# Optimization experiments

Measured on AMD Instinct MI355X. Metric: run time of the kernel, lower is better.

The kernel has to match this reference:

```python
import math
import jax, jax.numpy as jnp
import numpy as np

B, N, M, D, P, H, DH, L, FI = 4, 1024, 512, 512, 256, 8, 64, 6, 2048
ROT_DIM = 32          # min(32, dim_head)
NUM_BUCKETS, MAX_DIST = 32, 128


def layer_norm(x, g, stable=False, eps=1e-5):
    if stable:
        x = x / jax.lax.stop_gradient(jnp.max(x, axis=-1, keepdims=True))
    mu = jnp.mean(x, axis=-1, keepdims=True)
    var = jnp.mean(jnp.square(x - mu), axis=-1, keepdims=True)
    return (x - mu) * jax.lax.rsqrt(var + eps) * g


def rel_pos_bias(emb, i, j):
    # T5-style buckets for causal relative positions; emb: [NUM_BUCKETS, H]
    rel = jnp.arange(j)[None, :] - jnp.arange(i)[:, None]
    n = jnp.maximum(-rel, 0)
    max_exact = NUM_BUCKETS // 2
    nf = jnp.maximum(n, 1).astype(jnp.float32)
    large = max_exact + (jnp.log(nf / max_exact) / math.log(MAX_DIST / max_exact) * (NUM_BUCKETS - max_exact)).astype(jnp.int32)
    bucket = jnp.where(n < max_exact, n, jnp.minimum(large, NUM_BUCKETS - 1))
    return jnp.transpose(emb[bucket], (2, 0, 1))  # [h, i, j]


def rotary_pos(n):
    inv = 1.0 / (10000.0 ** (jnp.arange(0, ROT_DIM, 2, dtype=jnp.float32) / ROT_DIM))
    f = jnp.arange(n, dtype=jnp.float32)[:, None] * inv[None, :]
    return jnp.concatenate([f, f], axis=-1)  # [n, ROT_DIM]


def apply_rotary(pos, t):
    r = pos.shape[-1]
    t_rot, t_pass = t[..., :r], t[..., r:]
    x1, x2 = jnp.split(t_rot, 2, axis=-1)
    t_rot = t_rot * jnp.cos(pos) + jnp.concatenate([-x2, x1], axis=-1) * jnp.sin(pos)
    return jnp.concatenate([t_rot, t_pass], axis=-1)


def attention(x, kv_inp, norm_g, ctx_g, wq, wkv, null_kv, wo, out_g,
              attn_bias=None, causal=False, rot=None):
    b, n, _ = x.shape
    xn = layer_norm(x, norm_g)
    kv_in = xn if kv_inp is None else layer_norm(kv_inp, ctx_g)
    q = (xn @ wq).reshape(b, n, H, DH).transpose(0, 2, 1, 3)   # b h n d
    k, v = jnp.split(kv_in @ wkv, 2, axis=-1)                  # b m d (single-head kv)
    q = q * (DH ** -0.5)
    if rot is not None:
        q = apply_rotary(rot, q)
        k = apply_rotary(rot, k)
    k = jnp.concatenate([jnp.broadcast_to(null_kv[0], (b, 1, DH)), k], axis=1)
    v = jnp.concatenate([jnp.broadcast_to(null_kv[1], (b, 1, DH)), v], axis=1)
    sim = jnp.einsum('bhid,bjd->bhij', q, k)
    if attn_bias is not None:
        sim = sim + attn_bias
    if causal:
        i, j = sim.shape[-2], sim.shape[-1]
        mask = jnp.triu(jnp.ones((i, j), dtype=bool), j - i + 1)  # null token always visible
        sim = jnp.where(mask, jnp.finfo(sim.dtype).min, sim)
    attn = jax.nn.softmax(sim, axis=-1)
    out = jnp.einsum('bhij,bjd->bhid', attn, v).transpose(0, 2, 1, 3).reshape(b, n, H * DH)
    return layer_norm(out @ wo, out_g)


def feed_forward(x, g, w1, w2):
    h, gate = jnp.split(layer_norm(x, g) @ w1, 2, axis=-1)  # SwiGLU
    return (h * jax.nn.silu(gate)) @ w2


def _forward(x, context, rel_emb, sa_norm_g, sa_wq, sa_wkv, sa_null_kv, sa_wo, sa_out_g,
             ca_norm_g, ca_ctx_g, ca_wq, ca_wkv, ca_null_kv, ca_wo, ca_out_g,
             ff_norm_g, ff_w1, ff_w2, norm_g):
    n = x.shape[1]
    attn_bias = rel_pos_bias(rel_emb, n, n + 1)
    rot = rotary_pos(n)
    for l in range(sa_wq.shape[0]):
        x = attention(x, None, sa_norm_g[l], None, sa_wq[l], sa_wkv[l], sa_null_kv[l],
                      sa_wo[l], sa_out_g[l], attn_bias=attn_bias, causal=True, rot=rot) + x
        x = attention(x, context, ca_norm_g[l], ca_ctx_g[l], ca_wq[l], ca_wkv[l],
                      ca_null_kv[l], ca_wo[l], ca_out_g[l]) + x
        x = feed_forward(x, ff_norm_g[l], ff_w1[l], ff_w2[l]) + x
    return layer_norm(x, norm_g, stable=True)


def setup_inputs() -> dict:
    key = jax.random.key(0)
    ks = jax.random.split(key, 16)
    ID = H * DH
    r = lambda i, shape: jax.random.normal(ks[i], shape, jnp.float32) * 0.02
    return dict(
        x=jax.random.normal(ks[0], (B, N, D), jnp.float32),
        context=jax.random.normal(ks[1], (B, M, P), jnp.float32),
        rel_emb=r(2, (NUM_BUCKETS, H)),
        sa_norm_g=jnp.ones((L, D)), sa_wq=r(3, (L, D, ID)), sa_wkv=r(4, (L, D, 2 * DH)),
        sa_null_kv=r(5, (L, 2, DH)), sa_wo=r(6, (L, ID, D)), sa_out_g=jnp.ones((L, D)),
        ca_norm_g=jnp.ones((L, D)), ca_ctx_g=jnp.ones((L, P)), ca_wq=r(7, (L, D, ID)),
        ca_wkv=r(8, (L, P, 2 * DH)), ca_null_kv=r(9, (L, 2, DH)), ca_wo=r(10, (L, ID, D)),
        ca_out_g=jnp.ones((L, D)),
        ff_norm_g=jnp.ones((L, D)), ff_w1=r(11, (L, D, 2 * FI)), ff_w2=r(12, (L, FI, D)),
        norm_g=jnp.ones((D,)),
    )


def reference(x, context, rel_emb, sa_norm_g, sa_wq, sa_wkv, sa_null_kv, sa_wo, sa_out_g,
              ca_norm_g, ca_ctx_g, ca_wq, ca_wkv, ca_null_kv, ca_wo, ca_out_g,
              ff_norm_g, ff_w1, ff_w2, norm_g):
    return _forward(x, context, rel_emb, sa_norm_g, sa_wq, sa_wkv, sa_null_kv, sa_wo, sa_out_g,
                    ca_norm_g, ca_ctx_g, ca_wq, ca_wkv, ca_null_kv, ca_wo, ca_out_g,
                    ff_norm_g, ff_w1, ff_w2, norm_g)
```

## Files before the change

### kernel.cpp

```cpp
#include <hip/hip_runtime.h>
#include <hip/hip_bf16.h>
#include <math.h>

#define BB 4
#define NN 1024
#define MM 512
#define DD 512
#define PP 256
#define HH 8
#define DHH 64
#define LL 6
#define FFI 2048

typedef unsigned short u16;
typedef __attribute__((ext_vector_type(8))) short frag8;
typedef __attribute__((ext_vector_type(4))) float f32x4;

__device__ __forceinline__ u16 f2bf(float f) {
  union { float f; unsigned u; } x; x.f = f;
  unsigned u = x.u;
  return (u16)((u + 0x7FFFu + ((u >> 16) & 1u)) >> 16);
}

__global__ __launch_bounds__(256) void ln_kernel(const float* __restrict__ x,
                                                 const float* __restrict__ g,
                                                 const float* __restrict__ resid,
                                                 void* __restrict__ y,
                                                 int cols, int stable, int obf) {
  __shared__ float sbuf[8];
  int row = blockIdx.x;
  const float* xr = x + (size_t)row * cols;
  int tid = threadIdx.x;

  float inv_mx = 1.f;
  if (stable) {
    float mx = -INFINITY;
    for (int c = tid; c < cols; c += 256) mx = fmaxf(mx, xr[c]);
    #pragma unroll
    for (int o = 32; o > 0; o >>= 1) mx = fmaxf(mx, __shfl_xor(mx, o));
    if ((tid & 63) == 0) sbuf[tid >> 6] = mx;
    __syncthreads();
    mx = fmaxf(fmaxf(sbuf[0], sbuf[1]), fmaxf(sbuf[2], sbuf[3]));
    __syncthreads();
    inv_mx = 1.f / mx;
  }

  float sum = 0.f, ss = 0.f;
  for (int c = tid; c < cols; c += 256) {
    float v = xr[c] * inv_mx;
    sum += v; ss += v * v;
  }
  #pragma unroll
  for (int o = 32; o > 0; o >>= 1) { sum += __shfl_xor(sum, o); ss += __shfl_xor(ss, o); }
  if ((tid & 63) == 0) { sbuf[tid >> 6] = sum; sbuf[4 + (tid >> 6)] = ss; }
  __syncthreads();
  sum = sbuf[0] + sbuf[1] + sbuf[2] + sbuf[3];
  ss  = sbuf[4] + sbuf[5] + sbuf[6] + sbuf[7];

  float mean = sum / cols;
  float var  = ss / cols - mean * mean;
  float r = rsqrtf(var + 1e-5f);
  for (int c = tid; c < cols; c += 256) {
    float v = (xr[c] * inv_mx - mean) * r * g[c];
    if (resid) v += resid[(size_t)row * cols + c];
    if (obf) ((u16*)y)[(size_t)row * cols + c] = f2bf(v);
    else     ((float*)y)[(size_t)row * cols + c] = v;
  }
}

__global__ __launch_bounds__(256) void wtrans_kernel(const float* __restrict__ W,
                                                     u16* __restrict__ Wt,
                                                     int K, int N) {
  __shared__ float tile[32][33];
  size_t lofs = (size_t)blockIdx.z * K * N;
  const float* Wl = W + lofs;
  u16* Wtl = Wt + lofs;
  int n0 = blockIdx.x * 32, k0 = blockIdx.y * 32;
  int t = threadIdx.x;
  #pragma unroll
  for (int it = 0; it < 4; it++) {
    int idx = t + it * 256;
    int r = idx >> 5, c = idx & 31;
    tile[r][c] = Wl[(size_t)(k0 + r) * N + n0 + c];
  }
  __syncthreads();
  #pragma unroll
  for (int it = 0; it < 4; it++) {
    int idx = t + it * 256;
    int r = idx >> 5, c = idx & 31;
    Wtl[(size_t)(n0 + r) * K + k0 + c] = f2bf(tile[c][r]);
  }
}

#define LSTR 40

template<int TM, int TN, int RES>
__global__ __launch_bounds__(256) void mfma_gemm(const u16* __restrict__ A,
                                                 const u16* __restrict__ Bt,
                                                 float* __restrict__ C,
                                                 const float* __restrict__ res,
                                                 int M, int N, int K) {
  constexpr int TM2 = TM / 2, TN2 = TN / 2;
  constexpr int IT = TM2 / 16, JT = TN2 / 16;
  constexpr int ASLOT = TM * 4 / 256, BSLOT = TN * 4 / 256;
  __shared__ u16 As[TM * LSTR];
  __shared__ u16 Bs[TN * LSTR];
  int t = threadIdx.x;
  int w = t >> 6, lane = t & 63;
  int bm = blockIdx.y * TM, bn = blockIdx.x * TN;
  int wr = (w >> 1) * TM2, wc = (w & 1) * TN2;
  int lm = lane & 15, q = lane >> 4;

  f32x4 acc[IT][JT] = {};

  for (int k0 = 0; k0 < K; k0 += 32) {
    __syncthreads();
    #pragma unroll
    for (int i = 0; i < ASLOT; i++) {
      int s = t + i * 256; int m = s >> 2, c = s & 3;
      uint4 d = *(const uint4*)(A + (size_t)(bm + m) * K + k0 + c * 8);
      *(uint4*)&As[m * LSTR + c * 8] = d;
    }
    #pragma unroll
    for (int i = 0; i < BSLOT; i++) {
      int s = t + i * 256; int n = s >> 2, c = s & 3;
      uint4 d = *(const uint4*)(Bt + (size_t)(bn + n) * K + k0 + c * 8);
      *(uint4*)&Bs[n * LSTR + c * 8] = d;
    }
    __syncthreads();
    frag8 a[IT], b[JT];
    #pragma unroll
    for (int i = 0; i < IT; i++) a[i] = *(const frag8*)&As[(wr + i * 16 + lm) * LSTR + q * 8];
    #pragma unroll
    for (int j = 0; j < JT; j++) b[j] = *(const frag8*)&Bs[(wc + j * 16 + lm) * LSTR + q * 8];
    #pragma unroll
    for (int i = 0; i < IT; i++)
      #pragma unroll
      for (int j = 0; j < JT; j++)
        acc[i][j] = __builtin_amdgcn_mfma_f32_16x16x32_bf16(a[i], b[j], acc[i][j], 0, 0, 0);
  }

  #pragma unroll
  for (int i = 0; i < IT; i++)
    #pragma unroll
    for (int j = 0; j < JT; j++)
      #pragma unroll
      for (int r = 0; r < 4; r++) {
        int row = bm + wr + i * 16 + q * 4 + r;
        int col = bn + wc + j * 16 + lm;
        float v = acc[i][j][r];
        if (RES) v += res[(size_t)row * N + col];
        C[(size_t)row * N + col] = v;
      }
}

__global__ __launch_bounds__(256) void mfma_gemm_gated(const u16* __restrict__ A,
                                                       const u16* __restrict__ Bt,
                                                       u16* __restrict__ C,
                                                       int M, int FI, int K) {
  constexpr int TM = 128, TN = 64;
  constexpr int TM2 = 64, TN2 = 32;
  constexpr int IT = 4, JT = 2;
  __shared__ u16 As[TM * LSTR];
  __shared__ u16 Bh[TN * LSTR];
  __shared__ u16 Bg[TN * LSTR];
  int t = threadIdx.x;
  int w = t >> 6, lane = t & 63;
  int bm = blockIdx.y * TM, bn = blockIdx.x * TN;
  int wr = (w >> 1) * TM2, wc = (w & 1) * TN2;
  int lm = lane & 15, q = lane >> 4;

  f32x4 ah[IT][JT] = {};
  f32x4 ag[IT][JT] = {};

  for (int k0 = 0; k0 < K; k0 += 32) {
    __syncthreads();
    #pragma unroll
    for (int i = 0; i < 2; i++) {
      int s = t + i * 256; int m = s >> 2, c = s & 3;
      uint4 d = *(const uint4*)(A + (size_t)(bm + m) * K + k0 + c * 8);
      *(uint4*)&As[m * LSTR + c * 8] = d;
    }
    {
      int s = t; int n = s >> 2, c = s & 3;
      uint4 dh = *(const uint4*)(Bt + (size_t)(bn + n) * K + k0 + c * 8);
      uint4 dg = *(const uint4*)(Bt + (size_t)(bn + FI + n) * K + k0 + c * 8);
      *(uint4*)&Bh[n * LSTR + c * 8] = dh;
      *(uint4*)&Bg[n * LSTR + c * 8] = dg;
    }
    __syncthreads();
    frag8 a[IT], bh[JT], bg[JT];
    #pragma unroll
    for (int i = 0; i < IT; i++) a[i] = *(const frag8*)&As[(wr + i * 16 + lm) * LSTR + q * 8];
    #pragma unroll
    for (int j = 0; j < JT; j++) {
      bh[j] = *(const frag8*)&Bh[(wc + j * 16 + lm) * LSTR + q * 8];
      bg[j] = *(const frag8*)&Bg[(wc + j * 16 + lm) * LSTR + q * 8];
    }
    #pragma unroll
    for (int i = 0; i < IT; i++)
      #pragma unroll
      for (int j = 0; j < JT; j++) {
        ah[i][j] = __builtin_amdgcn_mfma_f32_16x16x32_bf16(a[i], bh[j], ah[i][j], 0, 0, 0);
        ag[i][j] = __builtin_amdgcn_mfma_f32_16x16x32_bf16(a[i], bg[j], ag[i][j], 0, 0, 0);
      }
  }

  #pragma unroll
  for (int i = 0; i < IT; i++)
    #pragma unroll
    for (int j = 0; j < JT; j++)
      #pragma unroll
      for (int r = 0; r < 4; r++) {
        int row = bm + wr + i * 16 + q * 4 + r;
        int col = bn + wc + j * 16 + lm;
        float h = ah[i][j][r], g = ag[i][j][r];
        float sg = 1.f / (1.f + __expf(-g));
        C[(size_t)row * FI + col] = f2bf(h * g * sg);
      }
}

__global__ __launch_bounds__(256) void biasprep_kernel(const float* __restrict__ rel_emb,
                                                       float* __restrict__ tab) {
  int idx = blockIdx.x * 256 + threadIdx.x;
  int h = idx >> 10, delta = idx & 1023;
  int bucket;
  if (delta < 16) bucket = delta;
  else {
    bucket = 16 + (int)(__logf((float)delta * (1.f / 16.f)) * (16.f / 2.0794415416798357f));
    if (bucket > 31) bucket = 31;
  }
  tab[idx] = rel_emb[bucket * HH + h];
}

__global__ __launch_bounds__(256) void qprep_kernel(const float* __restrict__ q_lin,
                                                    u16* __restrict__ q, int use_rot) {
  int idx = blockIdx.x * 256 + threadIdx.x;
  int d = idx & 63;
  int i = (idx >> 6) & 1023;
  int h = (idx >> 16) & 7;
  int b = idx >> 19;
  const float* src = q_lin + ((size_t)(b * NN + i)) * DD + h * DHH;
  float val = src[d] * 0.125f;
  if (use_rot && d < 32) {
    int dd = d & 15;
    float inv = powf(10000.f, -(float)dd * (1.f / 16.f));
    float a = (float)i * inv;
    float other = src[(d < 16) ? d + 16 : d - 16] * 0.125f;
    val = val * cosf(a) + ((d < 16) ? -other : other) * sinf(a);
  }
  q[idx] = f2bf(val);
}

__global__ __launch_bounds__(256) void kvprep_kernel(const float* __restrict__ kv_lin,
                                                     const float* __restrict__ null_kv,
                                                     u16* __restrict__ k, u16* __restrict__ vt,
                                                     int NK, int NKS, int NT, int use_rot) {
  int idx = blockIdx.x * 256 + threadIdx.x;
  int d = idx & 63;
  int rem = idx >> 6;
  int j = rem % NKS;
  int b = rem / NKS;
  float kval = 0.f, vval = 0.f;
  if (j == 0) {
    kval = null_kv[d];
    vval = null_kv[64 + d];
  } else if (j < NK) {
    int t = j - 1;
    const float* src = kv_lin + ((size_t)(b * NT + t)) * 128;
    kval = src[d];
    vval = src[64 + d];
    if (use_rot && d < 32) {
      int dd = d & 15;
      float inv = powf(10000.f, -(float)dd * (1.f / 16.f));
      float a = (float)t * inv;
      float other = src[(d < 16) ? d + 16 : d - 16];
      kval = kval * cosf(a) + ((d < 16) ? -other : other) * sinf(a);
    }
  }
  k[((size_t)b * NKS + j) * 64 + d] = f2bf(kval);
  vt[((size_t)b * 64 + d) * NKS + j] = f2bf(vval);
}

#define AT_STR 72

__global__ __launch_bounds__(256) void attn_mfma_kernel(
    const u16* __restrict__ q,
    const u16* __restrict__ kbuf,
    const u16* __restrict__ vtbuf,
    const float* __restrict__ bias_tab,
    u16* __restrict__ out,
    int n_keys, int NKS, int causal, int use_bias) {
  __shared__ u16 Ks[64 * AT_STR];
  __shared__ u16 Vts[64 * AT_STR];
  __shared__ u16 Sts[64 * AT_STR];
  __shared__ float bias_s[1024];

  int t = threadIdx.x;
  int wv = t >> 6, lane = t & 63;
  int lm = lane & 15, qd = lane >> 4;
  int bh = blockIdx.y;
  int b = bh >> 3, h = bh & 7;
  int i0 = blockIdx.x * 64;
  int wbase = wv * 16;

  if (use_bias) {
    *(float4*)&bias_s[t * 4] = *(const float4*)(bias_tab + h * 1024 + t * 4);
  }

  frag8 qf0, qf1;
  {
    const u16* qrow = q + ((size_t)bh * NN + i0 + wbase + lm) * 64 + qd * 8;
    qf0 = *(const frag8*)(qrow);
    qf1 = *(const frag8*)(qrow + 32);
  }

  float m_r[4], l_r[4];
  #pragma unroll
  for (int r = 0; r < 4; r++) { m_r[r] = -1e30f; l_r[r] = 0.f; }
  f32x4 of[4] = {};

  int num_t = causal ? (blockIdx.x + 2) : ((n_keys + 63) / 64);
  const u16* kb  = kbuf  + (size_t)b * NKS * 64;
  const u16* vtb = vtbuf + (size_t)b * 64 * NKS;

  for (int tile = 0; tile < num_t; tile++) {
    int j0 = tile * 64;
    __syncthreads();
    #pragma unroll
    for (int it = 0; it < 2; it++) {
      int pc = t + it * 256;
      int row = pc >> 3, seg = pc & 7;
      *(uint4*)&Ks[row * AT_STR + seg * 8] =
          *(const uint4*)(kb + (size_t)(j0 + row) * 64 + seg * 8);
      *(uint4*)&Vts[row * AT_STR + seg * 8] =
          *(const uint4*)(vtb + (size_t)row * NKS + j0 + seg * 8);
    }
    __syncthreads();

    f32x4 sf[4];
    #pragma unroll
    for (int jf = 0; jf < 4; jf++) {
      frag8 kf0 = *(const frag8*)&Ks[(jf * 16 + lm) * AT_STR + qd * 8];
      frag8 kf1 = *(const frag8*)&Ks[(jf * 16 + lm) * AT_STR + 32 + qd * 8];
      f32x4 sa = {};
      sa = __builtin_amdgcn_mfma_f32_16x16x32_bf16(qf0, kf0, sa, 0, 0, 0);
      sa = __builtin_amdgcn_mfma_f32_16x16x32_bf16(qf1, kf1, sa, 0, 0, 0);
      sf[jf] = sa;
    }

    float sv[4][4];
    float tmax[4] = {-1e30f, -1e30f, -1e30f, -1e30f};
    #pragma unroll
    for (int jf = 0; jf < 4; jf++) {
      int gj = j0 + jf * 16 + lm;
      #pragma unroll
      for (int r = 0; r < 4; r++) {
        int gi = i0 + wbase + qd * 4 + r;
        float val = sf[jf][r];
        if (use_bias) {
          int nd = gi - gj; nd = nd < 0 ? 0 : nd;
          val += bias_s[nd];
        }
        bool bad = (gj >= n_keys) || (causal && gj > gi + 1);
        val = bad ? -1e30f : val;
        sv[jf][r] = val;
        tmax[r] = fmaxf(tmax[r], val);
      }
    }
    #pragma unroll
    for (int r = 0; r < 4; r++) {
      tmax[r] = fmaxf(tmax[r], __shfl_xor(tmax[r], 1));
      tmax[r] = fmaxf(tmax[r], __shfl_xor(tmax[r], 2));
      tmax[r] = fmaxf(tmax[r], __shfl_xor(tmax[r], 4));
      tmax[r] = fmaxf(tmax[r], __shfl_xor(tmax[r], 8));
    }

    float alpha[4], rsum[4];
    #pragma unroll
    for (int r = 0; r < 4; r++) {
      float mn = fmaxf(m_r[r], tmax[r]);
      alpha[r] = __expf(m_r[r] - mn);
      m_r[r] = mn;
      rsum[r] = 0.f;
    }
    #pragma unroll
    for (int jf = 0; jf < 4; jf++) {
      #pragma unroll
      for (int r = 0; r < 4; r++) {
        float p = __expf(sv[jf][r] - m_r[r]);
        rsum[r] += p;
        Sts[(wbase + qd * 4 + r) * AT_STR + jf * 16 + lm] = f2bf(p);
      }
    }
    #pragma unroll
    for (int r = 0; r < 4; r++) {
      rsum[r] += __shfl_xor(rsum[r], 1);
      rsum[r] += __shfl_xor(rsum[r], 2);
      rsum[r] += __shfl_xor(rsum[r], 4);
      rsum[r] += __shfl_xor(rsum[r], 8);
      l_r[r] = l_r[r] * alpha[r] + rsum[r];
    }

    frag8 pf0 = *(const frag8*)&Sts[(wbase + lm) * AT_STR + qd * 8];
    frag8 pf1 = *(const frag8*)&Sts[(wbase + lm) * AT_STR + 32 + qd * 8];
    #pragma unroll
    for (int nf = 0; nf < 4; nf++) {
      f32x4 oc = of[nf];
      oc[0] *= alpha[0]; oc[1] *= alpha[1]; oc[2] *= alpha[2]; oc[3] *= alpha[3];
      frag8 vf0 = *(const frag8*)&Vts[(nf * 16 + lm) * AT_STR + qd * 8];
      frag8 vf1 = *(const frag8*)&Vts[(nf * 16 + lm) * AT_STR + 32 + qd * 8];
      oc = __builtin_amdgcn_mfma_f32_16x16x32_bf16(pf0, vf0, oc, 0, 0, 0);
      oc = __builtin_amdgcn_mfma_f32_16x16x32_bf16(pf1, vf1, oc, 0, 0, 0);
      of[nf] = oc;
    }
  }

  float invl[4];
  #pragma unroll
  for (int r = 0; r < 4; r++) invl[r] = 1.f / l_r[r];
  #pragma unroll
  for (int nf = 0; nf < 4; nf++)
    #pragma unroll
    for (int r = 0; r < 4; r++) {
      int gi = i0 + wbase + qd * 4 + r;
      out[((size_t)(b * NN + gi)) * DD + h * 64 + nf * 16 + lm] = f2bf(of[nf][r] * invl[r]);
    }
}

extern "C" void kernel_launch(void* const* d_in, const int* in_sizes, int n_in,
                              void* d_out, int out_size, void* d_ws, size_t ws_size,
                              hipStream_t stream) {
  const float* in_x      = (const float*)d_in[0];
  const float* in_ctx    = (const float*)d_in[1];
  const float* rel_emb   = (const float*)d_in[2];
  const float* sa_norm_g = (const float*)d_in[3];
  const float* sa_wq     = (const float*)d_in[4];
  const float* sa_wkv    = (const float*)d_in[5];
  const float* sa_nullkv = (const float*)d_in[6];
  const float* sa_wo     = (const float*)d_in[7];
  const float* sa_out_g  = (const float*)d_in[8];
  const float* ca_norm_g = (const float*)d_in[9];
  const float* ca_ctx_g  = (const float*)d_in[10];
  const float* ca_wq     = (const float*)d_in[11];
  const float* ca_wkv    = (const float*)d_in[12];
  const float* ca_nullkv = (const float*)d_in[13];
  const float* ca_wo     = (const float*)d_in[14];
  const float* ca_out_g  = (const float*)d_in[15];
  const float* ff_norm_g = (const float*)d_in[16];
  const float* ff_w1     = (const float*)d_in[17];
  const float* ff_w2     = (const float*)d_in[18];
  const float* norm_g    = (const float*)d_in[19];

  const size_t XSZ = (size_t)BB * NN * DD;
  const int NKS_SA = 1088;
  const int NKS_CA = 576;

  float* x_cur = (float*)d_out;

  char* p = (char*)d_ws;
  float* qlin     = (float*)p;  p += XSZ * 4;
  float* kvlin    = (float*)p;  p += (size_t)524288 * 4;
  float* bias_tab = (float*)p;  p += 8192 * 4;
  u16* xn_bf   = (u16*)p;  p += XSZ * 2;
  u16* ctxn_bf = (u16*)p;  p += (size_t)524288 * 2;
  u16* big_bf  = (u16*)p;  p += XSZ * 2;
  u16* ffh     = (u16*)p;  p += (size_t)8388608 * 2;
  u16* qbf     = (u16*)p;  p += XSZ * 2;
  u16* kbf     = (u16*)p;  p += (size_t)BB * NKS_SA * 64 * 2;
  u16* vtbf    = (u16*)p;  p += (size_t)BB * NKS_SA * 64 * 2;
  u16* wreg    = (u16*)p;

  const size_t S_WQ = 512 * 512, S_WKV = 512 * 128, S_WO = 512 * 512;
  const size_t S_CWQ = 512 * 512, S_CWKV = 256 * 128, S_CWO = 512 * 512;
  const size_t S_W1 = 512 * 4096, S_W2 = 2048 * 512;
  const size_t S_LAYER = S_WQ + S_WKV + S_WO + S_CWQ + S_CWKV + S_CWO + S_W1 + S_W2;

  const size_t base_bytes = (size_t)((char*)wreg - (char*)d_ws);
  const size_t need_all = base_bytes + (size_t)LL * S_LAYER * 2;
  const int all_mode = (ws_size >= need_all) ? 1 : 0;

  dim3 b256(256);

  biasprep_kernel<<<32, b256, 0, stream>>>(rel_emb, bias_tab);

  if (all_mode) {
    u16* pw = wreg;
    wtrans_kernel<<<dim3(16, 16, LL), b256, 0, stream>>>(sa_wq,  pw, 512, 512);  pw += LL * S_WQ;
    wtrans_kernel<<<dim3(4, 16, LL),  b256, 0, stream>>>(sa_wkv, pw, 512, 128);  pw += LL * S_WKV;
    wtrans_kernel<<<dim3(16, 16, LL), b256, 0, stream>>>(sa_wo,  pw, 512, 512);  pw += LL * S_WO;
    wtrans_kernel<<<dim3(16, 16, LL), b256, 0, stream>>>(ca_wq,  pw, 512, 512);  pw += LL * S_CWQ;
    wtrans_kernel<<<dim3(4, 8, LL),   b256, 0, stream>>>(ca_wkv, pw, 256, 128);  pw += LL * S_CWKV;
    wtrans_kernel<<<dim3(16, 16, LL), b256, 0, stream>>>(ca_wo,  pw, 512, 512);  pw += LL * S_CWO;
    wtrans_kernel<<<dim3(128, 16, LL),b256, 0, stream>>>(ff_w1,  pw, 512, 4096); pw += LL * S_W1;
    wtrans_kernel<<<dim3(16, 64, LL), b256, 0, stream>>>(ff_w2,  pw, 2048, 512);
  }

  hipMemcpyAsync(x_cur, in_x, sizeof(float) * XSZ, hipMemcpyDeviceToDevice, stream);

  const int ROWS = BB * NN;
  dim3 attn_grid(NN / 64, BB * HH);

  for (int l = 0; l < LL; l++) {
    const float* l_sa_norm = sa_norm_g + l * DD;
    const float* l_sa_null = sa_nullkv + l * 2 * DHH;
    const float* l_sa_outg = sa_out_g + l * DD;
    const float* l_ca_norm = ca_norm_g + l * DD;
    const float* l_ca_ctxg = ca_ctx_g + l * PP;
    const float* l_ca_null = ca_nullkv + l * 2 * DHH;
    const float* l_ca_outg = ca_out_g + l * DD;
    const float* l_ff_norm = ff_norm_g + l * DD;

    u16 *t_wq, *t_wkv, *t_wo, *t_cwq, *t_cwkv, *t_cwo, *t_w1, *t_w2;
    if (all_mode) {
      u16* pw = wreg;
      t_wq   = pw + l * S_WQ;   pw += LL * S_WQ;
      t_wkv  = pw + l * S_WKV;  pw += LL * S_WKV;
      t_wo   = pw + l * S_WO;   pw += LL * S_WO;
      t_cwq  = pw + l * S_CWQ;  pw += LL * S_CWQ;
      t_cwkv = pw + l * S_CWKV; pw += LL * S_CWKV;
      t_cwo  = pw + l * S_CWO;  pw += LL * S_CWO;
      t_w1   = pw + l * S_W1;   pw += LL * S_W1;
      t_w2   = pw + l * S_W2;
    } else {
      u16* pw = wreg;
      t_wq = pw;   pw += S_WQ;
      t_wkv = pw;  pw += S_WKV;
      t_wo = pw;   pw += S_WO;
      t_cwq = pw;  pw += S_CWQ;
      t_cwkv = pw; pw += S_CWKV;
      t_cwo = pw;  pw += S_CWO;
      t_w1 = pw;   pw += S_W1;
      t_w2 = pw;
      wtrans_kernel<<<dim3(16, 16, 1), b256, 0, stream>>>(sa_wq  + (size_t)l * S_WQ,   t_wq, 512, 512);
      wtrans_kernel<<<dim3(4, 16, 1),  b256, 0, stream>>>(sa_wkv + (size_t)l * S_WKV,  t_wkv, 512, 128);
      wtrans_kernel<<<dim3(16, 16, 1), b256, 0, stream>>>(sa_wo  + (size_t)l * S_WO,   t_wo, 512, 512);
      wtrans_kernel<<<dim3(16, 16, 1), b256, 0, stream>>>(ca_wq  + (size_t)l * S_CWQ,  t_cwq, 512, 512);
      wtrans_kernel<<<dim3(4, 8, 1),   b256, 0, stream>>>(ca_wkv + (size_t)l * S_CWKV, t_cwkv, 256, 128);
      wtrans_kernel<<<dim3(16, 16, 1), b256, 0, stream>>>(ca_wo  + (size_t)l * S_CWO,  t_cwo, 512, 512);
      wtrans_kernel<<<dim3(128, 16, 1),b256, 0, stream>>>(ff_w1  + (size_t)l * S_W1,   t_w1, 512, 4096);
      wtrans_kernel<<<dim3(16, 64, 1), b256, 0, stream>>>(ff_w2  + (size_t)l * S_W2,   t_w2, 2048, 512);
    }

    ln_kernel<<<ROWS, b256, 0, stream>>>(x_cur, l_sa_norm, nullptr, xn_bf, DD, 0, 1);
    mfma_gemm<128, 128, 0><<<dim3(4, 32), b256, 0, stream>>>(xn_bf, t_wq, qlin, nullptr, 4096, 512, 512);
    qprep_kernel<<<8192, b256, 0, stream>>>(qlin, qbf, 1);
    mfma_gemm<64, 64, 0><<<dim3(2, 64), b256, 0, stream>>>(xn_bf, t_wkv, kvlin, nullptr, 4096, 128, 512);
    kvprep_kernel<<<BB * NKS_SA / 4, b256, 0, stream>>>(kvlin, l_sa_null, kbf, vtbf, 1025, NKS_SA, 1024, 1);
    attn_mfma_kernel<<<attn_grid, b256, 0, stream>>>(qbf, kbf, vtbf, bias_tab, big_bf, 1025, NKS_SA, 1, 1);
    mfma_gemm<128, 128, 0><<<dim3(4, 32), b256, 0, stream>>>(big_bf, t_wo, qlin, nullptr, 4096, 512, 512);
    ln_kernel<<<ROWS, b256, 0, stream>>>(qlin, l_sa_outg, x_cur, x_cur, DD, 0, 0);

    ln_kernel<<<ROWS, b256, 0, stream>>>(x_cur, l_ca_norm, nullptr, xn_bf, DD, 0, 1);
    ln_kernel<<<BB * MM, b256, 0, stream>>>(in_ctx, l_ca_ctxg, nullptr, ctxn_bf, PP, 0, 1);
    mfma_gemm<128, 128, 0><<<dim3(4, 32), b256, 0, stream>>>(xn_bf, t_cwq, qlin, nullptr, 4096, 512, 512);
    qprep_kernel<<<8192, b256, 0, stream>>>(qlin, qbf, 0);
    mfma_gemm<64, 64, 0><<<dim3(2, 32), b256, 0, stream>>>(ctxn_bf, t_cwkv, kvlin, nullptr, 2048, 128, 256);
    kvprep_kernel<<<BB * NKS_CA / 4, b256, 0, stream>>>(kvlin, l_ca_null, kbf, vtbf, 513, NKS_CA, 512, 0);
    attn_mfma_kernel<<<attn_grid, b256, 0, stream>>>(qbf, kbf, vtbf, nullptr, big_bf, 513, NKS_CA, 0, 0);
    mfma_gemm<128, 128, 0><<<dim3(4, 32), b256, 0, stream>>>(big_bf, t_cwo, qlin, nullptr, 4096, 512, 512);
    ln_kernel<<<ROWS, b256, 0, stream>>>(qlin, l_ca_outg, x_cur, x_cur, DD, 0, 0);

    ln_kernel<<<ROWS, b256, 0, stream>>>(x_cur, l_ff_norm, nullptr, xn_bf, DD, 0, 1);
    mfma_gemm_gated<<<dim3(32, 32), b256, 0, stream>>>(xn_bf, t_w1, ffh, 4096, 2048, 512);
    mfma_gemm<128, 128, 1><<<dim3(4, 32), b256, 0, stream>>>(ffh, t_w2, x_cur, x_cur, 4096, 512, 2048);
  }

  ln_kernel<<<ROWS, b256, 0, stream>>>(x_cur, norm_g, nullptr, x_cur, DD, 1, 0);
}
```

Before: 2.027 ms.

## Fuse Q scaling/rotary into GEMM epilogue and restructure attention kernel

The Q projection GEMM gains an epilogue that applies the scale and rotary embedding and writes bf16 per-head Q directly, which removes the separate qprep kernel and its float round trip. The attention kernel moves to 32-row query tiles with 128 threads and computes S transposed (K·Q) so that each lane owns one query row. That layout lets the softmax reduction use two cross-lane shuffles instead of per-row reductions. It also register-prefetches the next K/V tile, applies masking only on boundary tiles, and reverses the causal block order so the heaviest blocks are scheduled first. The risks are more redundant K/V loads per query and lower per-block occupancy trade-offs.

```diff
diff --git a/kernel.cpp b/kernel.cpp
--- a/kernel.cpp
+++ b/kernel.cpp
@@ -94,12 +94,13 @@
 
 #define LSTR 40
 
-template<int TM, int TN, int RES>
+template<int TM, int TN, int RES, int QEPI>
 __global__ __launch_bounds__(256) void mfma_gemm(const u16* __restrict__ A,
                                                  const u16* __restrict__ Bt,
                                                  float* __restrict__ C,
                                                  const float* __restrict__ res,
-                                                 int M, int N, int K) {
+                                                 int M, int N, int K,
+                                                 u16* __restrict__ qout, int use_rot) {
   constexpr int TM2 = TM / 2, TN2 = TN / 2;
   constexpr int IT = TM2 / 16, JT = TN2 / 16;
   constexpr int ASLOT = TM * 4 / 256, BSLOT = TN * 4 / 256;
@@ -140,18 +141,44 @@
         acc[i][j] = __builtin_amdgcn_mfma_f32_16x16x32_bf16(a[i], b[j], acc[i][j], 0, 0, 0);
   }
 
-  #pragma unroll
-  for (int i = 0; i < IT; i++)
-    #pragma unroll
-    for (int j = 0; j < JT; j++)
+  if (QEPI) {
+    int h = (bn + wc) >> 6;
+    float invf = __powf(10000.f, -(float)lm * (1.f / 16.f));
+    #pragma unroll
+    for (int i = 0; i < IT; i++) {
       #pragma unroll
       for (int r = 0; r < 4; r++) {
         int row = bm + wr + i * 16 + q * 4 + r;
-        int col = bn + wc + j * 16 + lm;
-        float v = acc[i][j][r];
-        if (RES) v += res[(size_t)row * N + col];
-        C[(size_t)row * N + col] = v;
+        int b2 = row >> 10, n2 = row & 1023;
+        float vals[JT];
+        #pragma unroll
+        for (int j = 0; j < JT; j++) vals[j] = acc[i][j][r] * 0.125f;
+        if (use_rot) {
+          float a = (float)n2 * invf;
+          float s0 = sinf(a), c0 = cosf(a);
+          float v0 = vals[0], v1 = vals[1];
+          vals[0] = v0 * c0 - v1 * s0;
+          vals[1] = v1 * c0 + v0 * s0;
+        }
+        u16* dst = qout + (((size_t)(b2 * 8 + h) * 1024 + n2) << 6);
+        #pragma unroll
+        for (int j = 0; j < JT; j++) dst[j * 16 + lm] = f2bf(vals[j]);
       }
+    }
+  } else {
+    #pragma unroll
+    for (int i = 0; i < IT; i++)
+      #pragma unroll
+      for (int j = 0; j < JT; j++)
+        #pragma unroll
+        for (int r = 0; r < 4; r++) {
+          int row = bm + wr + i * 16 + q * 4 + r;
+          int col = bn + wc + j * 16 + lm;
+          float v = acc[i][j][r];
+          if (RES) v += res[(size_t)row * N + col];
+          C[(size_t)row * N + col] = v;
+        }
+  }
 }
 
 __global__ __launch_bounds__(256) void mfma_gemm_gated(const u16* __restrict__ A,
@@ -231,25 +258,6 @@
     if (bucket > 31) bucket = 31;
   }
   tab[idx] = rel_emb[bucket * HH + h];
-}
-
-__global__ __launch_bounds__(256) void qprep_kernel(const float* __restrict__ q_lin,
-                                                    u16* __restrict__ q, int use_rot) {
-  int idx = blockIdx.x * 256 + threadIdx.x;
-  int d = idx & 63;
-  int i = (idx >> 6) & 1023;
-  int h = (idx >> 16) & 7;
-  int b = idx >> 19;
-  const float* src = q_lin + ((size_t)(b * NN + i)) * DD + h * DHH;
-  float val = src[d] * 0.125f;
-  if (use_rot && d < 32) {
-    int dd = d & 15;
-    float inv = powf(10000.f, -(float)dd * (1.f / 16.f));
-    float a = (float)i * inv;
-    float other = src[(d < 16) ? d + 16 : d - 16] * 0.125f;
-    val = val * cosf(a) + ((d < 16) ? -other : other) * sinf(a);
-  }
-  q[idx] = f2bf(val);
 }
 
 __global__ __launch_bounds__(256) void kvprep_kernel(const float* __restrict__ kv_lin,
@@ -284,7 +292,7 @@
 
 #define AT_STR 72
 
-__global__ __launch_bounds__(256) void attn_mfma_kernel(
+__global__ __launch_bounds__(128) void attn_mfma_kernel(
     const u16* __restrict__ q,
     const u16* __restrict__ kbuf,
     const u16* __restrict__ vtbuf,
@@ -293,7 +301,7 @@
     int n_keys, int NKS, int causal, int use_bias) {
   __shared__ u16 Ks[64 * AT_STR];
   __shared__ u16 Vts[64 * AT_STR];
-  __shared__ u16 Sts[64 * AT_STR];
+  __shared__ u16 Sts[32 * AT_STR];
   __shared__ float bias_s[1024];
 
   int t = threadIdx.x;
@@ -301,40 +309,59 @@
   int lm = lane & 15, qd = lane >> 4;
   int bh = blockIdx.y;
   int b = bh >> 3, h = bh & 7;
-  int i0 = blockIdx.x * 64;
-  int wbase = wv * 16;
+  int bx = causal ? ((int)gridDim.x - 1 - (int)blockIdx.x) : (int)blockIdx.x;
+  int i0 = bx * 32;
 
   if (use_bias) {
-    *(float4*)&bias_s[t * 4] = *(const float4*)(bias_tab + h * 1024 + t * 4);
-  }
-
+    #pragma unroll
+    for (int it = 0; it < 2; it++)
+      *(float4*)&bias_s[(t + it * 128) * 4] =
+          *(const float4*)(bias_tab + h * 1024 + (t + it * 128) * 4);
+  }
+
+  int gi_row = i0 + wv * 16 + lm;
   frag8 qf0, qf1;
   {
-    const u16* qrow = q + ((size_t)bh * NN + i0 + wbase + lm) * 64 + qd * 8;
+    const u16* qrow = q + ((size_t)bh * NN + gi_row) * 64 + qd * 8;
     qf0 = *(const frag8*)(qrow);
     qf1 = *(const frag8*)(qrow + 32);
   }
 
-  float m_r[4], l_r[4];
-  #pragma unroll
-  for (int r = 0; r < 4; r++) { m_r[r] = -1e30f; l_r[r] = 0.f; }
+  float m_l = -1e30f, l_l = 0.f;
   f32x4 of[4] = {};
 
-  int num_t = causal ? (blockIdx.x + 2) : ((n_keys + 63) / 64);
+  int num_t = causal ? (((i0 + 32) >> 6) + 1) : ((n_keys + 63) >> 6);
   const u16* kb  = kbuf  + (size_t)b * NKS * 64;
   const u16* vtb = vtbuf + (size_t)b * 64 * NKS;
 
+  uint4 kreg[4], vreg[4];
+  #pragma unroll
+  for (int it = 0; it < 4; it++) {
+    int pc = t + it * 128;
+    int row = pc >> 3, seg = pc & 7;
+    kreg[it] = *(const uint4*)(kb + (size_t)row * 64 + seg * 8);
+    vreg[it] = *(const uint4*)(vtb + (size_t)row * NKS + seg * 8);
+  }
+
   for (int tile = 0; tile < num_t; tile++) {
-    int j0 = tile * 64;
-    __syncthreads();
-    #pragma unroll
-    for (int it = 0; it < 2; it++) {
-      int pc = t + it * 256;
+    int j0 = tile << 6;
+    __syncthreads();
+    #pragma unroll
+    for (int it = 0; it < 4; it++) {
+      int pc = t + it * 128;
       int row = pc >> 3, seg = pc & 7;
-      *(uint4*)&Ks[row * AT_STR + seg * 8] =
-          *(const uint4*)(kb + (size_t)(j0 + row) * 64 + seg * 8);
-      *(uint4*)&Vts[row * AT_STR + seg * 8] =
-          *(const uint4*)(vtb + (size_t)row * NKS + j0 + seg * 8);
+      *(uint4*)&Ks[row * AT_STR + seg * 8]  = kreg[it];
+      *(uint4*)&Vts[row * AT_STR + seg * 8] = vreg[it];
+    }
+    if (tile + 1 < num_t) {
+      int j1 = j0 + 64;
+      #pragma unroll
+      for (int it = 0; it < 4; it++) {
+        int pc = t + it * 128;
+        int row = pc >> 3, seg = pc & 7;
+        kreg[it] = *(const uint4*)(kb + (size_t)(j1 + row) * 64 + seg * 8);
+        vreg[it] = *(const uint4*)(vtb + (size_t)row * NKS + j1 + seg * 8);
+      }
     }
     __syncthreads();
 
@@ -344,70 +371,65 @@
       frag8 kf0 = *(const frag8*)&Ks[(jf * 16 + lm) * AT_STR + qd * 8];
       frag8 kf1 = *(const frag8*)&Ks[(jf * 16 + lm) * AT_STR + 32 + qd * 8];
       f32x4 sa = {};
-      sa = __builtin_amdgcn_mfma_f32_16x16x32_bf16(qf0, kf0, sa, 0, 0, 0);
-      sa = __builtin_amdgcn_mfma_f32_16x16x32_bf16(qf1, kf1, sa, 0, 0, 0);
+      sa = __builtin_amdgcn_mfma_f32_16x16x32_bf16(kf0, qf0, sa, 0, 0, 0);
+      sa = __builtin_amdgcn_mfma_f32_16x16x32_bf16(kf1, qf1, sa, 0, 0, 0);
       sf[jf] = sa;
     }
 
+    bool mtile = causal ? (j0 + 62 > i0) : (j0 + 63 >= n_keys);
     float sv[4][4];
-    float tmax[4] = {-1e30f, -1e30f, -1e30f, -1e30f};
+    float mx = -1e30f;
     #pragma unroll
     for (int jf = 0; jf < 4; jf++) {
-      int gj = j0 + jf * 16 + lm;
       #pragma unroll
       for (int r = 0; r < 4; r++) {
-        int gi = i0 + wbase + qd * 4 + r;
+        int gj = j0 + jf * 16 + qd * 4 + r;
         float val = sf[jf][r];
         if (use_bias) {
-          int nd = gi - gj; nd = nd < 0 ? 0 : nd;
+          int nd = gi_row - gj; nd = nd < 0 ? 0 : nd;
           val += bias_s[nd];
         }
-        bool bad = (gj >= n_keys) || (causal && gj > gi + 1);
-        val = bad ? -1e30f : val;
+        if (mtile) {
+          bool bad = causal ? (gj > gi_row + 1) : (gj >= n_keys);
+          val = bad ? -1e30f : val;
+        }
         sv[jf][r] = val;
-        tmax[r] = fmaxf(tmax[r], val);
+        mx = fmaxf(mx, val);
       }
     }
-    #pragma unroll
-    for (int r = 0; r < 4; r++) {
-      tmax[r] = fmaxf(tmax[r], __shfl_xor(tmax[r], 1));
-      tmax[r] = fmaxf(tmax[r], __shfl_xor(tmax[r], 2));
-      tmax[r] = fmaxf(tmax[r], __shfl_xor(tmax[r], 4));
-      tmax[r] = fmaxf(tmax[r], __shfl_xor(tmax[r], 8));
-    }
-
-    float alpha[4], rsum[4];
-    #pragma unroll
-    for (int r = 0; r < 4; r++) {
-      float mn = fmaxf(m_r[r], tmax[r]);
-      alpha[r] = __expf(m_r[r] - mn);
-      m_r[r] = mn;
-      rsum[r] = 0.f;
-    }
+    mx = fmaxf(mx, __shfl_xor(mx, 16));
+    mx = fmaxf(mx, __shfl_xor(mx, 32));
+
+    float m_new = fmaxf(m_l, mx);
+    float alpha = __expf(m_l - m_new);
+    m_l = m_new;
+    float sum = 0.f;
     #pragma unroll
     for (int jf = 0; jf < 4; jf++) {
-      #pragma unroll
-      for (int r = 0; r < 4; r++) {
-        float p = __expf(sv[jf][r] - m_r[r]);
-        rsum[r] += p;
-        Sts[(wbase + qd * 4 + r) * AT_STR + jf * 16 + lm] = f2bf(p);
-      }
-    }
-    #pragma unroll
-    for (int r = 0; r < 4; r++) {
-      rsum[r] += __shfl_xor(rsum[r], 1);
-      rsum[r] += __shfl_xor(rsum[r], 2);
-      rsum[r] += __shfl_xor(rsum[r], 4);
-      rsum[r] += __shfl_xor(rsum[r], 8);
-      l_r[r] = l_r[r] * alpha[r] + rsum[r];
-    }
-
-    frag8 pf0 = *(const frag8*)&Sts[(wbase + lm) * AT_STR + qd * 8];
-    frag8 pf1 = *(const frag8*)&Sts[(wbase + lm) * AT_STR + 32 + qd * 8];
+      float p0 = __expf(sv[jf][0] - m_new);
+      float p1 = __expf(sv[jf][1] - m_new);
+      float p2 = __expf(sv[jf][2] - m_new);
+      float p3 = __expf(sv[jf][3] - m_new);
+      sum += (p0 + p1) + (p2 + p3);
+      unsigned p01 = (unsigned)f2bf(p0) | ((unsigned)f2bf(p1) << 16);
+      unsigned p23 = (unsigned)f2bf(p2) | ((unsigned)f2bf(p3) << 16);
+      *(uint2*)&Sts[(wv * 16 + lm) * AT_STR + jf * 16 + qd * 4] = make_uint2(p01, p23);
+    }
+    sum += __shfl_xor(sum, 16);
+    sum += __shfl_xor(sum, 32);
+    l_l = l_l * alpha + sum;
+
+    float aR0 = __shfl(alpha, qd * 4 + 0);
+    float aR1 = __shfl(alpha, qd * 4 + 1);
+    float aR2 = __shfl(alpha, qd * 4 + 2);
+    float aR3 = __shfl(alpha, qd * 4 + 3);
+
+    frag8 pf0 = *(const frag8*)&Sts[(wv * 16 + lm) * AT_STR + qd * 8];
+    frag8 pf1 = *(const frag8*)&Sts[(wv * 16 + lm) * AT_STR + 32 + qd * 8];
     #pragma unroll
     for (int nf = 0; nf < 4; nf++) {
       f32x4 oc = of[nf];
-      oc[0] *= alpha[0]; oc[1] *= alpha[1]; oc[2] *= alpha[2]; oc[3] *= alpha[3];
+      oc[0] *= aR0; oc[1] *= aR1; oc[2] *= aR2; oc[3] *= aR3;
       frag8 vf0 = *(const frag8*)&Vts[(nf * 16 + lm) * AT_STR + qd * 8];
       frag8 vf1 = *(const frag8*)&Vts[(nf * 16 + lm) * AT_STR + 32 + qd * 8];
       oc = __builtin_amdgcn_mfma_f32_16x16x32_bf16(pf0, vf0, oc, 0, 0, 0);
@@ -416,15 +438,18 @@
     }
   }
 
-  float invl[4];
-  #pragma unroll
-  for (int r = 0; r < 4; r++) invl[r] = 1.f / l_r[r];
+  float invl = 1.f / l_l;
+  float iR[4];
+  iR[0] = __shfl(invl, qd * 4 + 0);
+  iR[1] = __shfl(invl, qd * 4 + 1);
+  iR[2] = __shfl(invl, qd * 4 + 2);
+  iR[3] = __shfl(invl, qd * 4 + 3);
   #pragma unroll
   for (int nf = 0; nf < 4; nf++)
     #pragma unroll
     for (int r = 0; r < 4; r++) {
-      int gi = i0 + wbase + qd * 4 + r;
-      out[((size_t)(b * NN + gi)) * DD + h * 64 + nf * 16 + lm] = f2bf(of[nf][r] * invl[r]);
+      int gi = i0 + wv * 16 + qd * 4 + r;
+      out[((size_t)(b * NN + gi)) * DD + h * 64 + nf * 16 + lm] = f2bf(of[nf][r] * iR[r]);
     }
 }
 
@@ -499,7 +524,7 @@
   hipMemcpyAsync(x_cur, in_x, sizeof(float) * XSZ, hipMemcpyDeviceToDevice, stream);
 
   const int ROWS = BB * NN;
-  dim3 attn_grid(NN / 64, BB * HH);
+  dim3 attn_grid(NN / 32, BB * HH);
 
   for (int l = 0; l < LL; l++) {
     const float* l_sa_norm = sa_norm_g + l * DD;
@@ -543,27 +568,25 @@
     }
 
     ln_kernel<<<ROWS, b256, 0, stream>>>(x_cur, l_sa_norm, nullptr, xn_bf, DD, 0, 1);
-    mfma_gemm<128, 128, 0><<<dim3(4, 32), b256, 0, stream>>>(xn_bf, t_wq, qlin, nullptr, 4096, 512, 512);
-    qprep_kernel<<<8192, b256, 0, stream>>>(qlin, qbf, 1);
-    mfma_gemm<64, 64, 0><<<dim3(2, 64), b256, 0, stream>>>(xn_bf, t_wkv, kvlin, nullptr, 4096, 128, 512);
+    mfma_gemm<128, 128, 0, 1><<<dim3(4, 32), b256, 0, stream>>>(xn_bf, t_wq, qlin, nullptr, 4096, 512, 512, qbf, 1);
+    mfma_gemm<64, 64, 0, 0><<<dim3(2, 64), b256, 0, stream>>>(xn_bf, t_wkv, kvlin, nullptr, 4096, 128, 512, nullptr, 0);
     kvprep_kernel<<<BB * NKS_SA / 4, b256, 0, stream>>>(kvlin, l_sa_null, kbf, vtbf, 1025, NKS_SA, 1024, 1);
-    attn_mfma_kernel<<<attn_grid, b256, 0, stream>>>(qbf, kbf, vtbf, bias_tab, big_bf, 1025, NKS_SA, 1, 1);
-    mfma_gemm<128, 128, 0><<<dim3(4, 32), b256, 0, stream>>>(big_bf, t_wo, qlin, nullptr, 4096, 512, 512);
+    attn_mfma_kernel<<<attn_grid, 128, 0, stream>>>(qbf, kbf, vtbf, bias_tab, big_bf, 1025, NKS_SA, 1, 1);
+    mfma_gemm<128, 128, 0, 0><<<dim3(4, 32), b256, 0, stream>>>(big_bf, t_wo, qlin, nullptr, 4096, 512, 512, nullptr, 0);
     ln_kernel<<<ROWS, b256, 0, stream>>>(qlin, l_sa_outg, x_cur, x_cur, DD, 0, 0);
 
     ln_kernel<<<ROWS, b256, 0, stream>>>(x_cur, l_ca_norm, nullptr, xn_bf, DD, 0, 1);
     ln_kernel<<<BB * MM, b256, 0, stream>>>(in_ctx, l_ca_ctxg, nullptr, ctxn_bf, PP, 0, 1);
-    mfma_gemm<128, 128, 0><<<dim3(4, 32), b256, 0, stream>>>(xn_bf, t_cwq, qlin, nullptr, 4096, 512, 512);
-    qprep_kernel<<<8192, b256, 0, stream>>>(qlin, qbf, 0);
-    mfma_gemm<64, 64, 0><<<dim3(2, 32), b256, 0, stream>>>(ctxn_bf, t_cwkv, kvlin, nullptr, 2048, 128, 256);
+    mfma_gemm<128, 128, 0, 1><<<dim3(4, 32), b256, 0, stream>>>(xn_bf, t_cwq, qlin, nullptr, 4096, 512, 512, qbf, 0);
+    mfma_gemm<64, 64, 0, 0><<<dim3(2, 32), b256, 0, stream>>>(ctxn_bf, t_cwkv, kvlin, nullptr, 2048, 128, 256, nullptr, 0);
     kvprep_kernel<<<BB * NKS_CA / 4, b256, 0, stream>>>(kvlin, l_ca_null, kbf, vtbf, 513, NKS_CA, 512, 0);
-    attn_mfma_kernel<<<attn_grid, b256, 0, stream>>>(qbf, kbf, vtbf, nullptr, big_bf, 513, NKS_CA, 0, 0);
-    mfma_gemm<128, 128, 0><<<dim3(4, 32), b256, 0, stream>>>(big_bf, t_cwo, qlin, nullptr, 4096, 512, 512);
+    attn_mfma_kernel<<<attn_grid, 128, 0, stream>>>(qbf, kbf, vtbf, nullptr, big_bf, 513, NKS_CA, 0, 0);
+    mfma_gemm<128, 128, 0, 0><<<dim3(4, 32), b256, 0, stream>>>(big_bf, t_cwo, qlin, nullptr, 4096, 512, 512, nullptr, 0);
     ln_kernel<<<ROWS, b256, 0, stream>>>(qlin, l_ca_outg, x_cur, x_cur, DD, 0, 0);
 
     ln_kernel<<<ROWS, b256, 0, stream>>>(x_cur, l_ff_norm, nullptr, xn_bf, DD, 0, 1);
     mfma_gemm_gated<<<dim3(32, 32), b256, 0, stream>>>(xn_bf, t_w1, ffh, 4096, 2048, 512);
-    mfma_gemm<128, 128, 1><<<dim3(4, 32), b256, 0, stream>>>(ffh, t_w2, x_cur, x_cur, 4096, 512, 2048);
+    mfma_gemm<128, 128, 1, 0><<<dim3(4, 32), b256, 0, stream>>>(ffh, t_w2, x_cur, x_cur, 4096, 512, 2048, nullptr, 0);
   }
 
   ln_kernel<<<ROWS, b256, 0, stream>>>(x_cur, norm_g, nullptr, x_cur, DD, 1, 0);
```

Result: slower. 2.239 ms (+10.5%).
